# Kernel tuning notes

Measured on AMD Instinct MI355X. Metric: run time of the kernel, lower is better.

## Reference

```python
import jax, jax.numpy as jnp
import numpy as np

TOP_K = 4
N_GROUP = 8
TOPK_GROUP = 4
SCALE = 1.0

B, S, H, I, E = 2, 1024, 1024, 512, 32
SHARED_I = I * 2  # n_shared_experts = 2


def setup_inputs() -> dict:
    key = jax.random.key(0)
    ks = jax.random.split(key, 9)
    return {
        "hidden_states": jax.random.normal(ks[0], (B, S, H), jnp.float32),
        "gate_w": jax.random.normal(ks[1], (E, H), jnp.float32) * 0.02,
        "gate_bias": jnp.zeros((E,), jnp.float32),
        "gate_proj": jax.random.normal(ks[2], (E, I, H), jnp.float32) * 0.02,
        "up_proj": jax.random.normal(ks[3], (E, I, H), jnp.float32) * 0.02,
        "down_proj": jax.random.normal(ks[4], (E, H, I), jnp.float32) * 0.02,
        "shared_gate_w": jax.random.normal(ks[5], (SHARED_I, H), jnp.float32) * 0.02,
        "shared_up_w": jax.random.normal(ks[6], (SHARED_I, H), jnp.float32) * 0.02,
        "shared_down_w": jax.random.normal(ks[7], (H, SHARED_I), jnp.float32) * 0.02,
    }


def reference(hidden_states, gate_w, gate_bias, gate_proj, up_proj, down_proj,
              shared_gate_w, shared_up_w, shared_down_w):
    b, s, h = hidden_states.shape
    e = gate_w.shape[0]
    x = hidden_states.reshape(-1, h)            # (T, H)
    t = x.shape[0]

    # ---- gating (DeepSeek-V3 grouped sigmoid routing) ----
    logits = x @ gate_w.T                       # (T, E)
    scores = jax.nn.sigmoid(logits)
    sfc = scores + gate_bias[None, :]           # scores_for_choice
    # per-group score = sum of top-2 experts in group
    group_scores = jax.lax.top_k(sfc.reshape(t, N_GROUP, -1), 2)[0].sum(-1)  # (T, G)
    _, gidx = jax.lax.top_k(group_scores, TOPK_GROUP)                        # (T, topk_group)
    gmask = jax.nn.one_hot(gidx, N_GROUP, dtype=sfc.dtype).sum(1)            # (T, G)
    smask = jnp.repeat(gmask, e // N_GROUP, axis=1)                          # (T, E)
    tmp = jnp.where(smask > 0, sfc, 0.0)
    _, topk_idx = jax.lax.top_k(tmp, TOP_K)                                  # (T, K)
    topk_w = jnp.take_along_axis(scores, topk_idx, axis=1)                   # (T, K)
    topk_w = topk_w / (topk_w.sum(-1, keepdims=True) + 1e-20)                # norm_topk_prob
    topk_w = topk_w * SCALE

    # ---- routed experts (dense combine-weight formulation) ----
    comb = jnp.zeros((t, e), x.dtype).at[jnp.arange(t)[:, None], topk_idx].add(topk_w)  # (T, E)
    g = jnp.einsum('th,eih->eti', x, gate_proj)   # (E, T, I)
    u = jnp.einsum('th,eih->eti', x, up_proj)     # (E, T, I)
    a = jax.nn.silu(g) * u
    a = a * comb.T[:, :, None]                    # scale before down-proj to skip zero experts
    out = jnp.einsum('eti,ehi->th', a, down_proj) # (T, H)

    # ---- shared experts ----
    sg = x @ shared_gate_w.T
    su = x @ shared_up_w.T
    out = out + (jax.nn.silu(sg) * su) @ shared_down_w.T

    return out.reshape(b, s, h)
```

## Files before the change

kernel.cpp:

```cpp
#include <hip/hip_runtime.h>
#include <hip/hip_bf16.h>
#include <cstdint>
#include <cstddef>

#define H_DIM 1024
#define I_DIM 512
#define E_NUM 32
#define SHARED_I_DIM 1024
#define TOPK 4
#define NGROUP 8
#define TOPKG 4
#define GT 8

typedef __attribute__((ext_vector_type(8))) short bf16x8;
typedef __attribute__((ext_vector_type(4))) float f32x4;
typedef __attribute__((ext_vector_type(8))) unsigned short u16x8;

__device__ inline unsigned short f2bf(float f) {
    __hip_bfloat16 h = __float2bfloat16(f);
    return *reinterpret_cast<unsigned short*>(&h);
}
__device__ inline float bf2f(unsigned short u) {
    union { unsigned int u; float f; } w;
    w.u = ((unsigned int)u) << 16;
    return w.f;
}

__device__ inline void bar_lds() {
    asm volatile("s_waitcnt lgkmcnt(0)" ::: "memory");
    __builtin_amdgcn_s_barrier();
}

__device__ inline int laddr32(int row, int chunk) {
    return row * 32 + (((chunk) ^ (row & 3)) << 3);
}

__global__ void init_kernel(int* cnt) {
    if (threadIdx.x < 64) cnt[threadIdx.x] = 0;
}

__global__ void cvt_kernel(const float* __restrict__ src, unsigned short* __restrict__ dst, int n8) {
    int i = blockIdx.x * blockDim.x + threadIdx.x;
    if (i >= n8) return;
    float4 a = *(const float4*)(src + (size_t)i * 8);
    float4 b = *(const float4*)(src + (size_t)i * 8 + 4);
    u16x8 v;
    v[0] = f2bf(a.x); v[1] = f2bf(a.y); v[2] = f2bf(a.z); v[3] = f2bf(a.w);
    v[4] = f2bf(b.x); v[5] = f2bf(b.y); v[6] = f2bf(b.z); v[7] = f2bf(b.w);
    *(u16x8*)(dst + (size_t)i * 8) = v;
}

__global__ __launch_bounds__(256) void gate_kernel(const float* __restrict__ x,
                                                   const float* __restrict__ gw,
                                                   float* __restrict__ logits_out) {
    int tb = blockIdx.x;
    int tid = threadIdx.x;
    __shared__ float xs[GT][H_DIM];
    __shared__ float ps[8][GT][E_NUM];
    const float* xsrc = x + (size_t)tb * GT * H_DIM;
    for (int i = tid; i < GT * H_DIM / 4; i += 256)
        ((float4*)&xs[0][0])[i] = ((const float4*)xsrc)[i];
    __syncthreads();
    int e = tid & 31, part = tid >> 5;
    const float* wrow = gw + (size_t)e * H_DIM + part * 128;
    float acc[GT] = {};
    for (int c0 = 0; c0 < 128; c0 += 32) {
        float w[32];
#pragma unroll
        for (int c = 0; c < 32; c++) w[c] = wrow[c0 + c];
#pragma unroll
        for (int t = 0; t < GT; t++) {
#pragma unroll
            for (int c = 0; c < 32; c++)
                acc[t] += w[c] * xs[t][part * 128 + c0 + c];
        }
    }
#pragma unroll
    for (int t = 0; t < GT; t++) ps[part][t][e] = acc[t];
    __syncthreads();
    {
        int t = tid >> 5, ee = tid & 31;
        float s = 0.f;
#pragma unroll
        for (int p = 0; p < 8; p++) s += ps[p][t][ee];
        logits_out[((size_t)tb * GT + t) * E_NUM + ee] = s;
    }
}

__global__ void select_kernel(const float* __restrict__ logits, const float* __restrict__ gb,
                              int* __restrict__ topk_e, float* __restrict__ topk_w,
                              int* __restrict__ cnt, int T) {
    int t = blockIdx.x * blockDim.x + threadIdx.x;
    if (t >= T) return;
    float scores[E_NUM], sfc[E_NUM];
#pragma unroll
    for (int i = 0; i < E_NUM; i++) {
        float l = logits[(size_t)t * E_NUM + i];
        float s = 1.f / (1.f + expf(-l));
        scores[i] = s;
        sfc[i] = s + gb[i];
    }
    float gs[NGROUP];
#pragma unroll
    for (int g = 0; g < NGROUP; g++) {
        float m1 = -1e30f, m2 = -1e30f;
#pragma unroll
        for (int j = 0; j < 4; j++) {
            float v = sfc[g * 4 + j];
            if (v > m1) { m2 = m1; m1 = v; }
            else if (v > m2) { m2 = v; }
        }
        gs[g] = m1 + m2;
    }
    unsigned gmask = 0;
    for (int r = 0; r < TOPKG; r++) {
        int best = 0; float bv = -1e30f;
#pragma unroll
        for (int g = 0; g < NGROUP; g++)
            if (!((gmask >> g) & 1u) && gs[g] > bv) { bv = gs[g]; best = g; }
        gmask |= 1u << best;
    }
    unsigned cmask = 0;
    int eidx[TOPK]; float ew[TOPK]; float sum = 0.f;
    for (int r = 0; r < TOPK; r++) {
        int best = 0; float bv = -1e30f; float bsc = 0.f;
#pragma unroll
        for (int i = 0; i < E_NUM; i++) {
            float v = ((gmask >> (i >> 2)) & 1u) ? sfc[i] : 0.0f;
            if (!((cmask >> i) & 1u) && v > bv) { bv = v; best = i; bsc = scores[i]; }
        }
        cmask |= 1u << best;
        eidx[r] = best; ew[r] = bsc; sum += bsc;
    }
    float inv = 1.f / (sum + 1e-20f);
#pragma unroll
    for (int k = 0; k < TOPK; k++) {
        topk_e[t * TOPK + k] = eidx[k];
        topk_w[t * TOPK + k] = ew[k] * inv;
        atomicAdd(&cnt[eidx[k]], 1);
    }
}

__global__ void scan_kernel(const int* __restrict__ cnt, int* __restrict__ off) {
    if (threadIdx.x == 0) {
        int a = 0;
        for (int e = 0; e < E_NUM; e++) { off[e] = a; a += cnt[e]; }
        off[E_NUM] = a;
    }
}

__global__ void bin_kernel(const int* __restrict__ topk_e, const float* __restrict__ topk_w,
                           const int* __restrict__ off, int* __restrict__ cnt2,
                           int* __restrict__ slot_token, float* __restrict__ slot_w,
                           int* __restrict__ slot_of, int total) {
    int i = blockIdx.x * blockDim.x + threadIdx.x;
    if (i >= total) return;
    int e = topk_e[i];
    float w = topk_w[i];
    int pos = atomicAdd(&cnt2[e], 1);
    int slot = off[e] + pos;
    slot_token[slot] = i >> 2;
    slot_w[slot] = w;
    slot_of[i] = slot;
}

__global__ __launch_bounds__(256) void combine_kernel(const unsigned short* __restrict__ out_slot,
                                                      const int* __restrict__ slot_of,
                                                      float* __restrict__ out) {
    int t = blockIdx.x;
    int h = threadIdx.x * 4;
    int s0 = slot_of[t * TOPK + 0], s1 = slot_of[t * TOPK + 1];
    int s2 = slot_of[t * TOPK + 2], s3 = slot_of[t * TOPK + 3];
    ushort4 a = *(const ushort4*)(out_slot + (size_t)s0 * H_DIM + h);
    ushort4 b = *(const ushort4*)(out_slot + (size_t)s1 * H_DIM + h);
    ushort4 c = *(const ushort4*)(out_slot + (size_t)s2 * H_DIM + h);
    ushort4 d = *(const ushort4*)(out_slot + (size_t)s3 * H_DIM + h);
    float4 o = *(float4*)(out + (size_t)t * H_DIM + h);
    o.x += bf2f(a.x) + bf2f(b.x) + bf2f(c.x) + bf2f(d.x);
    o.y += bf2f(a.y) + bf2f(b.y) + bf2f(c.y) + bf2f(d.y);
    o.z += bf2f(a.z) + bf2f(b.z) + bf2f(c.z) + bf2f(d.z);
    o.w += bf2f(a.w) + bf2f(b.w) + bf2f(c.w) + bf2f(d.w);
    *(float4*)(out + (size_t)t * H_DIM + h) = o;
}

template <bool STAGE1>
__global__ __launch_bounds__(512, 2) void moe_gemm(
    const unsigned short* __restrict__ Axr, const unsigned short* __restrict__ Axs,
    const float* __restrict__ B1r_, const float* __restrict__ B2r_,
    const float* __restrict__ B1s_, const float* __restrict__ B2s_,
    void* __restrict__ Dr, void* __restrict__ Ds,
    const int* __restrict__ slot_token, const float* __restrict__ slot_w,
    const int* __restrict__ cnt, const int* __restrict__ off_arr, int T) {
    constexpr bool DUAL = STAGE1;
    int e = blockIdx.x, itile = blockIdx.y, mtile = blockIdx.z;
    bool sh = (e == E_NUM);
    int NI = (STAGE1 && !sh) ? (I_DIM / 64) : 16;
    if (itile >= NI) return;
    int count = sh ? T : cnt[e];
    int base = sh ? 0 : off_arr[e];
    if (mtile * 256 >= count) return;
    const int K = STAGE1 ? H_DIM : (sh ? SHARED_I_DIM : I_DIM);

    __shared__ __align__(16) unsigned short LA[2][256 * 32];
    __shared__ __align__(16) unsigned short LB1[2][64 * 32];
    __shared__ __align__(16) unsigned short LB2[2][DUAL ? 64 * 32 : 8];

    int tid = threadIdx.x;
    int as_row = tid >> 1, asub = tid & 1;
    int am = mtile * 256 + as_row;
    int amc = (am < count) ? am : 0;
    const unsigned short* Arow;
    if constexpr (STAGE1) {
        int tok = sh ? amc : slot_token[base + amc];
        Arow = Axr + (size_t)tok * H_DIM + asub * 16;
    } else {
        Arow = sh ? (Axs + (size_t)amc * SHARED_I_DIM + asub * 16)
                  : (Axr + (size_t)(base + amc) * I_DIM + asub * 16);
    }
    int half = tid >> 8;
    int bt = tid & 255;
    int b_row = bt >> 2, b_ch = bt & 3;
    int brow = itile * 64 + b_row;
    const float* Bsrc;
    if constexpr (STAGE1) {
        if (sh) Bsrc = (half ? B2s_ : B1s_) + (size_t)brow * K + b_ch * 8;
        else    Bsrc = (half ? B2r_ : B1r_) + (size_t)e * (I_DIM * H_DIM) + (size_t)brow * K + b_ch * 8;
    } else {
        Bsrc = sh ? (B1s_ + (size_t)brow * K + b_ch * 8)
                  : (B1r_ + (size_t)e * (H_DIM * I_DIM) + (size_t)brow * K + b_ch * 8);
    }
    const bool doB = DUAL || (half == 0);

    f32x4 acc1[4][2] = {};
    f32x4 acc2[DUAL ? 4 : 1][2] = {};

    int lane = tid & 63, wid = tid >> 6;
    int wrow = (wid >> 1) * 64, wcol = (wid & 1) * 32;
    int frow = lane & 15, fch = lane >> 4;

    u16x8 pA0[2], pA1[2];
    float4 blo0, bhi0, blo1, bhi1;

    auto loadS = [&](u16x8* pA, float4& blo, float4& bhi, int k0) {
        pA[0] = *(const u16x8*)(Arow + k0);
        pA[1] = *(const u16x8*)(Arow + k0 + 8);
        if (doB) {
            blo = *(const float4*)(Bsrc + k0);
            bhi = *(const float4*)(Bsrc + k0 + 4);
        }
    };
    auto writeS = [&](int buf, const u16x8* pA, float4 blo, float4 bhi) {
        *(u16x8*)(&LA[buf][laddr32(as_row, asub * 2)]) = pA[0];
        *(u16x8*)(&LA[buf][laddr32(as_row, asub * 2 + 1)]) = pA[1];
        if (doB) {
            u16x8 s;
            s[0] = f2bf(blo.x); s[1] = f2bf(blo.y); s[2] = f2bf(blo.z); s[3] = f2bf(blo.w);
            s[4] = f2bf(bhi.x); s[5] = f2bf(bhi.y); s[6] = f2bf(bhi.z); s[7] = f2bf(bhi.w);
            unsigned short* d = (DUAL && half) ? &LB2[buf][0] : &LB1[buf][0];
            *(u16x8*)(&d[laddr32(b_row, b_ch)]) = s;
        }
    };
    auto compute = [&](int buf) {
        bf16x8 af[4], bf1[2], bf2[DUAL ? 2 : 1];
#pragma unroll
        for (int nf = 0; nf < 2; nf++)
            bf1[nf] = *(const bf16x8*)(&LB1[buf][laddr32(wcol + nf * 16 + frow, fch)]);
        if constexpr (DUAL) {
#pragma unroll
            for (int nf = 0; nf < 2; nf++)
                bf2[nf] = *(const bf16x8*)(&LB2[buf][laddr32(wcol + nf * 16 + frow, fch)]);
        }
#pragma unroll
        for (int mf = 0; mf < 4; mf++)
            af[mf] = *(const bf16x8*)(&LA[buf][laddr32(wrow + mf * 16 + frow, fch)]);
#pragma unroll
        for (int mf = 0; mf < 4; mf++)
#pragma unroll
            for (int nf = 0; nf < 2; nf++) {
                acc1[mf][nf] = __builtin_amdgcn_mfma_f32_16x16x32_bf16(af[mf], bf1[nf], acc1[mf][nf], 0, 0, 0);
                if constexpr (DUAL)
                    acc2[mf][nf] = __builtin_amdgcn_mfma_f32_16x16x32_bf16(af[mf], bf2[nf], acc2[mf][nf], 0, 0, 0);
            }
    };

    const int NK = K >> 5;
    loadS(pA0, blo0, bhi0, 0);
    loadS(pA1, blo1, bhi1, 32);
    writeS(0, pA0, blo0, bhi0);
    loadS(pA0, blo0, bhi0, 64);
    bar_lds();
    for (int it = 0; it < NK; it += 2) {
        writeS(1, pA1, blo1, bhi1);
        if (it + 3 < NK) loadS(pA1, blo1, bhi1, (it + 3) << 5);
        compute(0);
        bar_lds();
        if (it + 2 < NK) {
            writeS(0, pA0, blo0, bhi0);
            if (it + 4 < NK) loadS(pA0, blo0, bhi0, (it + 4) << 5);
        }
        compute(1);
        if (it + 2 < NK) bar_lds();
    }

#pragma unroll
    for (int mf = 0; mf < 4; mf++)
#pragma unroll
        for (int nf = 0; nf < 2; nf++)
#pragma unroll
            for (int j = 0; j < 4; j++) {
                int rloc = wrow + mf * 16 + (lane >> 4) * 4 + j;
                int mrow = mtile * 256 + rloc;
                int col = itile * 64 + wcol + nf * 16 + (lane & 15);
                if (mrow >= count) continue;
                if constexpr (STAGE1) {
                    float w = sh ? 1.0f : slot_w[base + mrow];
                    float g = acc1[mf][nf][j];
                    float a = (g / (1.f + __expf(-g))) * acc2[mf][nf][j] * w;
                    if (sh) ((unsigned short*)Ds)[(size_t)mrow * SHARED_I_DIM + col] = f2bf(a);
                    else    ((unsigned short*)Dr)[(size_t)(base + mrow) * I_DIM + col] = f2bf(a);
                } else {
                    if (sh) ((float*)Ds)[(size_t)mrow * H_DIM + col] = acc1[mf][nf][j];
                    else    ((unsigned short*)Dr)[(size_t)(base + mrow) * H_DIM + col] = f2bf(acc1[mf][nf][j]);
                }
            }
}

extern "C" void kernel_launch(void* const* d_in, const int* in_sizes, int n_in,
                              void* d_out, int out_size, void* d_ws, size_t ws_size,
                              hipStream_t stream) {
    const float* x = (const float*)d_in[0];
    const float* gw = (const float*)d_in[1];
    const float* gb = (const float*)d_in[2];
    const float* gate_proj = (const float*)d_in[3];
    const float* up_proj = (const float*)d_in[4];
    const float* down_proj = (const float*)d_in[5];
    const float* sgw = (const float*)d_in[6];
    const float* suw = (const float*)d_in[7];
    const float* sdw = (const float*)d_in[8];
    float* out = (float*)d_out;

    const int T = in_sizes[0] / H_DIM;
    const int total_slots = T * TOPK;

    char* ws = (char*)d_ws;
    int* cnt = (int*)ws;
    int* cnt2 = cnt + 32;
    int* off = cnt + 64;
    int* topk_e = cnt + 128;
    float* topk_w = (float*)(topk_e + total_slots);
    int* slot_token = (int*)(topk_w + total_slots);
    float* slot_w = (float*)(slot_token + total_slots);
    int* slot_of = (int*)(slot_w + total_slots);
    float* logits = (float*)(slot_of + total_slots);
    unsigned short* x_bf = (unsigned short*)(logits + (size_t)T * E_NUM);
    unsigned short* act_r = x_bf + (size_t)T * H_DIM;
    unsigned short* act_s = act_r + (size_t)(total_slots + 256) * I_DIM;
    unsigned short* out_slot = act_s + (size_t)T * SHARED_I_DIM;

    hipLaunchKernelGGL(init_kernel, dim3(1), dim3(64), 0, stream, cnt);
    hipLaunchKernelGGL(cvt_kernel, dim3((T * H_DIM / 8 + 255) / 256), dim3(256), 0, stream,
                       x, x_bf, T * H_DIM / 8);
    hipLaunchKernelGGL(gate_kernel, dim3(T / GT), dim3(256), 0, stream, x, gw, logits);
    hipLaunchKernelGGL(select_kernel, dim3((T + 255) / 256), dim3(256), 0, stream,
                       logits, gb, topk_e, topk_w, cnt, T);
    hipLaunchKernelGGL(scan_kernel, dim3(1), dim3(1), 0, stream, cnt, off);
    hipLaunchKernelGGL(bin_kernel, dim3((total_slots + 255) / 256), dim3(256), 0, stream,
                       topk_e, topk_w, off, cnt2, slot_token, slot_w, slot_of, total_slots);

    hipLaunchKernelGGL((moe_gemm<true>), dim3(E_NUM + 1, 16, 16), dim3(512), 0, stream,
                       x_bf, (const unsigned short*)nullptr,
                       gate_proj, up_proj, sgw, suw,
                       (void*)act_r, (void*)act_s,
                       slot_token, slot_w, cnt, off, T);

    hipLaunchKernelGGL((moe_gemm<false>), dim3(E_NUM + 1, 16, 16), dim3(512), 0, stream,
                       act_r, act_s,
                       down_proj, (const float*)nullptr, sdw, (const float*)nullptr,
                       (void*)out_slot, (void*)out,
                       slot_token, slot_w, cnt, off, T);

    hipLaunchKernelGGL(combine_kernel, dim3(T), dim3(256), 0, stream, out_slot, slot_of, out);
}
```

Baseline: 211.7 us.

## Stage GEMM tiles with direct global-to-LDS loads and convert B at read

Replaces the register-staged A/B prefetch and explicit LDS stores with global_load_lds DMA copies straight into shared memory, using new swizzle patterns for A (bf16) and B (kept as fp32 in LDS). The bf16 conversion of weights now happens when fragments are read from LDS instead of before the LDS store. The loop becomes a simple one-ahead double buffer with __syncthreads. This cuts VGPR staging and store instructions, but doubles LDS footprint and traffic for B and repeats the conversion in every wave that reads the same B rows.

```diff
diff --git a/kernel.cpp b/kernel.cpp
--- a/kernel.cpp
+++ b/kernel.cpp
@@ -26,13 +26,10 @@
     return w.f;
 }
 
-__device__ inline void bar_lds() {
-    asm volatile("s_waitcnt lgkmcnt(0)" ::: "memory");
-    __builtin_amdgcn_s_barrier();
-}
-
-__device__ inline int laddr32(int row, int chunk) {
-    return row * 32 + (((chunk) ^ (row & 3)) << 3);
+__device__ inline void gload16(const void* g, void* lds) {
+    __builtin_amdgcn_global_load_lds(
+        (const __attribute__((address_space(1))) void*)g,
+        (__attribute__((address_space(3))) void*)lds, 16, 0, 0);
 }
 
 __global__ void init_kernel(int* cnt) {
@@ -202,104 +199,107 @@
     const int K = STAGE1 ? H_DIM : (sh ? SHARED_I_DIM : I_DIM);
 
     __shared__ __align__(16) unsigned short LA[2][256 * 32];
-    __shared__ __align__(16) unsigned short LB1[2][64 * 32];
-    __shared__ __align__(16) unsigned short LB2[2][DUAL ? 64 * 32 : 8];
-
-    int tid = threadIdx.x;
-    int as_row = tid >> 1, asub = tid & 1;
-    int am = mtile * 256 + as_row;
-    int amc = (am < count) ? am : 0;
-    const unsigned short* Arow;
+    __shared__ __align__(16) float LB1[2][64 * 32];
+    __shared__ __align__(16) float LB2[DUAL ? 2 : 1][DUAL ? 64 * 32 : 4];
+
+    int tid = threadIdx.x, lane = tid & 63, wid = tid >> 6;
+
+    int r0 = wid * 32 + (lane >> 2);
+    int r1 = r0 + 16;
+    const unsigned short* Abase = STAGE1 ? Axr : (sh ? Axs : Axr);
+    size_t arow0, arow1;
+    {
+        int am0 = mtile * 256 + r0, am1 = mtile * 256 + r1;
+        int amc0 = (am0 < count) ? am0 : 0, amc1 = (am1 < count) ? am1 : 0;
+        if constexpr (STAGE1) {
+            arow0 = sh ? (size_t)amc0 : (size_t)slot_token[base + amc0];
+            arow1 = sh ? (size_t)amc1 : (size_t)slot_token[base + amc1];
+        } else {
+            arow0 = sh ? (size_t)amc0 : (size_t)(base + amc0);
+            arow1 = sh ? (size_t)amc1 : (size_t)(base + amc1);
+        }
+    }
+    const unsigned short* gA0 = Abase + arow0 * K + (((lane & 3) ^ ((r0 >> 1) & 3)) << 3);
+    const unsigned short* gA1 = Abase + arow1 * K + (((lane & 3) ^ ((r1 >> 1) & 3)) << 3);
+    unsigned short* lA0 = &LA[0][(wid * 32) * 32];
+    unsigned short* lA1 = &LA[0][(wid * 32 + 16) * 32];
+    const int ABUF = 256 * 32;
+
+    int br = wid * 8 + (lane >> 3);
+    int brow = itile * 64 + br;
+    int cb = (lane & 7) ^ (br & 7);
+    const float* gB1;
+    const float* gB2 = nullptr;
     if constexpr (STAGE1) {
-        int tok = sh ? amc : slot_token[base + amc];
-        Arow = Axr + (size_t)tok * H_DIM + asub * 16;
+        gB1 = (sh ? B1s_ : (B1r_ + (size_t)e * I_DIM * H_DIM)) + (size_t)brow * K + cb * 4;
+        gB2 = (sh ? B2s_ : (B2r_ + (size_t)e * I_DIM * H_DIM)) + (size_t)brow * K + cb * 4;
     } else {
-        Arow = sh ? (Axs + (size_t)amc * SHARED_I_DIM + asub * 16)
-                  : (Axr + (size_t)(base + amc) * I_DIM + asub * 16);
-    }
-    int half = tid >> 8;
-    int bt = tid & 255;
-    int b_row = bt >> 2, b_ch = bt & 3;
-    int brow = itile * 64 + b_row;
-    const float* Bsrc;
-    if constexpr (STAGE1) {
-        if (sh) Bsrc = (half ? B2s_ : B1s_) + (size_t)brow * K + b_ch * 8;
-        else    Bsrc = (half ? B2r_ : B1r_) + (size_t)e * (I_DIM * H_DIM) + (size_t)brow * K + b_ch * 8;
-    } else {
-        Bsrc = sh ? (B1s_ + (size_t)brow * K + b_ch * 8)
-                  : (B1r_ + (size_t)e * (H_DIM * I_DIM) + (size_t)brow * K + b_ch * 8);
-    }
-    const bool doB = DUAL || (half == 0);
+        gB1 = (sh ? B1s_ : (B1r_ + (size_t)e * H_DIM * I_DIM)) + (size_t)brow * K + cb * 4;
+    }
+    float* lB1 = &LB1[0][(wid * 8) * 32];
+    float* lB2 = DUAL ? &LB2[0][(wid * 8) * 32] : nullptr;
+    const int BBUF = 64 * 32;
 
     f32x4 acc1[4][2] = {};
     f32x4 acc2[DUAL ? 4 : 1][2] = {};
 
-    int lane = tid & 63, wid = tid >> 6;
     int wrow = (wid >> 1) * 64, wcol = (wid & 1) * 32;
     int frow = lane & 15, fch = lane >> 4;
 
-    u16x8 pA0[2], pA1[2];
-    float4 blo0, bhi0, blo1, bhi1;
-
-    auto loadS = [&](u16x8* pA, float4& blo, float4& bhi, int k0) {
-        pA[0] = *(const u16x8*)(Arow + k0);
-        pA[1] = *(const u16x8*)(Arow + k0 + 8);
-        if (doB) {
-            blo = *(const float4*)(Bsrc + k0);
-            bhi = *(const float4*)(Bsrc + k0 + 4);
-        }
+    auto STAGE = [&](int buf, int it) {
+        int k0 = it << 5;
+        gload16(gA0 + k0, lA0 + buf * ABUF);
+        gload16(gA1 + k0, lA1 + buf * ABUF);
+        gload16(gB1 + k0, lB1 + buf * BBUF);
+        if constexpr (DUAL) gload16(gB2 + k0, lB2 + buf * BBUF);
     };
-    auto writeS = [&](int buf, const u16x8* pA, float4 blo, float4 bhi) {
-        *(u16x8*)(&LA[buf][laddr32(as_row, asub * 2)]) = pA[0];
-        *(u16x8*)(&LA[buf][laddr32(as_row, asub * 2 + 1)]) = pA[1];
-        if (doB) {
-            u16x8 s;
-            s[0] = f2bf(blo.x); s[1] = f2bf(blo.y); s[2] = f2bf(blo.z); s[3] = f2bf(blo.w);
-            s[4] = f2bf(bhi.x); s[5] = f2bf(bhi.y); s[6] = f2bf(bhi.z); s[7] = f2bf(bhi.w);
-            unsigned short* d = (DUAL && half) ? &LB2[buf][0] : &LB1[buf][0];
-            *(u16x8*)(&d[laddr32(b_row, b_ch)]) = s;
-        }
+
+    auto rdB = [&](const float* Bb, int nf) -> bf16x8 {
+        int r = wcol + nf * 16 + frow;
+        f32x4 lo = *(const f32x4*)(Bb + r * 32 + ((((fch << 1)) ^ (r & 7)) << 2));
+        f32x4 hi = *(const f32x4*)(Bb + r * 32 + ((((fch << 1) + 1) ^ (r & 7)) << 2));
+        u16x8 s;
+        s[0] = f2bf(lo[0]); s[1] = f2bf(lo[1]); s[2] = f2bf(lo[2]); s[3] = f2bf(lo[3]);
+        s[4] = f2bf(hi[0]); s[5] = f2bf(hi[1]); s[6] = f2bf(hi[2]); s[7] = f2bf(hi[3]);
+        union { u16x8 u; bf16x8 b; } cvt; cvt.u = s;
+        return cvt.b;
     };
+
     auto compute = [&](int buf) {
-        bf16x8 af[4], bf1[2], bf2[DUAL ? 2 : 1];
-#pragma unroll
-        for (int nf = 0; nf < 2; nf++)
-            bf1[nf] = *(const bf16x8*)(&LB1[buf][laddr32(wcol + nf * 16 + frow, fch)]);
+        const unsigned short* As_ = &LA[buf][0];
+        const float* B1_ = &LB1[buf][0];
+        bf16x8 af[4], b1[2], b2[DUAL ? 2 : 1];
+#pragma unroll
+        for (int nf = 0; nf < 2; nf++) b1[nf] = rdB(B1_, nf);
         if constexpr (DUAL) {
-#pragma unroll
-            for (int nf = 0; nf < 2; nf++)
-                bf2[nf] = *(const bf16x8*)(&LB2[buf][laddr32(wcol + nf * 16 + frow, fch)]);
+            const float* B2_ = &LB2[buf][0];
+#pragma unroll
+            for (int nf = 0; nf < 2; nf++) b2[nf] = rdB(B2_, nf);
+        }
+#pragma unroll
+        for (int mf = 0; mf < 4; mf++) {
+            int r = wrow + mf * 16 + frow;
+            af[mf] = *(const bf16x8*)(As_ + r * 32 + ((fch ^ ((r >> 1) & 3)) << 3));
         }
 #pragma unroll
         for (int mf = 0; mf < 4; mf++)
-            af[mf] = *(const bf16x8*)(&LA[buf][laddr32(wrow + mf * 16 + frow, fch)]);
-#pragma unroll
-        for (int mf = 0; mf < 4; mf++)
 #pragma unroll
             for (int nf = 0; nf < 2; nf++) {
-                acc1[mf][nf] = __builtin_amdgcn_mfma_f32_16x16x32_bf16(af[mf], bf1[nf], acc1[mf][nf], 0, 0, 0);
+                acc1[mf][nf] = __builtin_amdgcn_mfma_f32_16x16x32_bf16(af[mf], b1[nf], acc1[mf][nf], 0, 0, 0);
                 if constexpr (DUAL)
-                    acc2[mf][nf] = __builtin_amdgcn_mfma_f32_16x16x32_bf16(af[mf], bf2[nf], acc2[mf][nf], 0, 0, 0);
+                    acc2[mf][nf] = __builtin_amdgcn_mfma_f32_16x16x32_bf16(af[mf], b2[nf], acc2[mf][nf], 0, 0, 0);
             }
     };
 
     const int NK = K >> 5;
-    loadS(pA0, blo0, bhi0, 0);
-    loadS(pA1, blo1, bhi1, 32);
-    writeS(0, pA0, blo0, bhi0);
-    loadS(pA0, blo0, bhi0, 64);
-    bar_lds();
-    for (int it = 0; it < NK; it += 2) {
-        writeS(1, pA1, blo1, bhi1);
-        if (it + 3 < NK) loadS(pA1, blo1, bhi1, (it + 3) << 5);
-        compute(0);
-        bar_lds();
-        if (it + 2 < NK) {
-            writeS(0, pA0, blo0, bhi0);
-            if (it + 4 < NK) loadS(pA0, blo0, bhi0, (it + 4) << 5);
-        }
-        compute(1);
-        if (it + 2 < NK) bar_lds();
+    STAGE(0, 0);
+    __syncthreads();
+    int buf = 0;
+    for (int it = 0; it < NK; ++it) {
+        if (it + 1 < NK) STAGE(buf ^ 1, it + 1);
+        compute(buf);
+        __syncthreads();
+        buf ^= 1;
     }
 
 #pragma unroll
```

Measured after the change: 207.6 us. No clear change (-1.9%).
